# Kernel tuning notes

Measured on AMD Instinct MI355X. Metric: run time of the kernel, lower is better.

Reference implementation:

```python
import jax, jax.numpy as jnp
from jax import lax
import numpy as np

C_IN, D_INNER, D_STATE, OUT_CH = 20, 32, 8, 20
DT_RANK = max(1, D_INNER // 8)
B, H, W = 4, 384, 384
EPS = 1e-5


def layernorm(x, g, b):
    m = jnp.mean(x, axis=-1, keepdims=True)
    v = jnp.mean((x - m) ** 2, axis=-1, keepdims=True)
    return (x - m) * lax.rsqrt(v + EPS) * g + b


def ss1d(x, xw, dw, db, A_log, Dp):
    # x: (Bb, L, Dd). Mamba selective scan: h_t = exp(dt*A)*h_{t-1} + dt*B_t*u_t; y_t = C_t.h_t + D*u_t
    Bb, L, Dd = x.shape
    N = A_log.shape[1]
    xdbl = x @ xw.T                                   # (Bb, L, dtr+2N)
    dt_lo, Bm, Cm = jnp.split(xdbl, [DT_RANK, DT_RANK + N], axis=-1)
    dt = jax.nn.softplus(dt_lo @ dw.T + db)           # (Bb, L, Dd)
    A = -jnp.exp(A_log)                               # (Dd, N)

    def step(h, inp):
        dt_t, B_t, C_t, u_t = inp                     # (Bb,Dd),(Bb,N),(Bb,N),(Bb,Dd)
        dA = jnp.exp(dt_t[:, :, None] * A)            # (Bb, Dd, N)
        h = dA * h + (dt_t * u_t)[:, :, None] * B_t[:, None, :]
        y = jnp.einsum('bdn,bn->bd', h, C_t)
        return h, y

    xs = (jnp.moveaxis(dt, 1, 0), jnp.moveaxis(Bm, 1, 0),
          jnp.moveaxis(Cm, 1, 0), jnp.moveaxis(x, 1, 0))
    h0 = jnp.zeros((Bb, Dd, N), dtype=x.dtype)
    _, ys = lax.scan(step, h0, xs)
    return jnp.moveaxis(ys, 0, 1) + x * Dp


def setup_inputs() -> dict:
    key = jax.random.key(0)
    ks = jax.random.split(key, 16)
    s = lambda k, shp, sc=0.05: jax.random.normal(k, shp, dtype=jnp.float32) * sc
    A_log1 = jnp.log(jnp.broadcast_to(jnp.arange(1, D_STATE + 1, dtype=jnp.float32), (D_INNER, D_STATE)))
    return {
        'x': jax.random.normal(ks[0], (B, C_IN, H, W), dtype=jnp.float32),
        'norm_g': jnp.ones((C_IN,), jnp.float32),
        'norm_b': jnp.zeros((C_IN,), jnp.float32),
        'inproj_w': s(ks[1], (D_INNER, C_IN), 0.15),
        'dw_w': s(ks[2], (3, 3, 1, D_INNER), 0.2),
        'dw_b': jnp.zeros((D_INNER,), jnp.float32),
        'ssm_xw': s(ks[3], (4, DT_RANK + 2 * D_STATE, D_INNER), 0.1),
        'ssm_dw': s(ks[4], (4, D_INNER, DT_RANK), 0.5),
        'ssm_db': s(ks[5], (4, D_INNER), 0.5) - 3.0,
        'ssm_Alog': jnp.broadcast_to(A_log1, (4, D_INNER, D_STATE)).copy(),
        'ssm_D': jnp.ones((4, D_INNER), jnp.float32),
        'merge_g': jnp.ones((4 * D_INNER,), jnp.float32),
        'merge_b': jnp.zeros((4 * D_INNER,), jnp.float32),
        'merge_w': s(ks[6], (D_INNER, 4 * D_INNER), 0.1),
        'out_w': s(ks[7], (OUT_CH, D_INNER), 0.15),
        'out_b': jnp.zeros((OUT_CH,), jnp.float32),
    }


def reference(x, norm_g, norm_b, inproj_w, dw_w, dw_b, ssm_xw, ssm_dw, ssm_db,
              ssm_Alog, ssm_D, merge_g, merge_b, merge_w, out_w, out_b):
    Bx, C, Hx, Wx = x.shape
    h = jnp.transpose(x, (0, 2, 3, 1))                      # (B,H,W,C)
    h = layernorm(h, norm_g, norm_b)
    h = jax.nn.silu(h @ inproj_w.T)                          # (B,H,W,Dd)
    h = lax.conv_general_dilated(h, dw_w, (1, 1), 'SAME',
                                 dimension_numbers=('NHWC', 'HWIO', 'NHWC'),
                                 feature_group_count=D_INNER) + dw_b
    h = jax.nn.silu(h)                                       # (B,H,W,Dd)

    p = lambda i: (ssm_xw[i], ssm_dw[i], ssm_db[i], ssm_Alog[i], ssm_D[i])

    x_h = h.reshape(Bx * Hx, Wx, D_INNER)
    y_h_fwd = ss1d(x_h, *p(0)).reshape(Bx, Hx, Wx, D_INNER)
    y_h_bwd = ss1d(x_h[:, ::-1], *p(1))[:, ::-1].reshape(Bx, Hx, Wx, D_INNER)

    x_v = jnp.transpose(h, (0, 2, 1, 3)).reshape(Bx * Wx, Hx, D_INNER)
    y_v_fwd = jnp.transpose(ss1d(x_v, *p(2)).reshape(Bx, Wx, Hx, D_INNER), (0, 2, 1, 3))
    y_v_bwd = jnp.transpose(ss1d(x_v[:, ::-1], *p(3))[:, ::-1].reshape(Bx, Wx, Hx, D_INNER), (0, 2, 1, 3))

    y = jnp.concatenate([y_h_fwd, y_h_bwd, y_v_fwd, y_v_bwd], axis=-1)  # (B,H,W,4*Dd)
    y = layernorm(y, merge_g, merge_b)
    y = y @ merge_w.T                                        # (B,H,W,Dd)
    y = y @ out_w.T + out_b                                  # (B,H,W,out_ch)
    return jnp.transpose(y, (0, 3, 1, 2))                    # (B,out_ch,H,W)
```

## Files before the change

kernel.cpp:

```cpp
#include <hip/hip_runtime.h>

typedef unsigned short u16;
typedef unsigned int   u32;
typedef unsigned long long u64;
typedef float f2 __attribute__((ext_vector_type(2)));

#define CIN  20
#define DIN  32
#define BB   4
#define HH   384
#define WW   384
#define HW   147456
#define BHW  589824
#define EPSF 1e-5f
#define GUARD 65536

__device__ __forceinline__ float bflo(u32 u) {
    union { u32 v; float f; } x; x.v = u << 16; return x.f;
}
__device__ __forceinline__ float bfhi(u32 u) {
    union { u32 v; float f; } x; x.v = u & 0xffff0000u; return x.f;
}
__device__ __forceinline__ float bf2f(u16 h) {
    union { u32 v; float f; } x; x.v = ((u32)h) << 16; return x.f;
}
__device__ __forceinline__ u16 f2bf(float f) {
    union { float f; u32 u; } v; v.f = f;
    u32 u = v.u;
    return (u16)((u + 0x7FFFu + ((u >> 16) & 1u)) >> 16);
}
__device__ __forceinline__ float silu_f(float a) {
    return a / (1.f + __expf(-a));
}
__device__ __forceinline__ float softplus_f(float z) {
    return (z > 15.f) ? z : __logf(1.f + __expf(z));
}

__global__ void k_prep(const float* __restrict__ ow, const float* __restrict__ mw,
                       const float* __restrict__ mg, const float* __restrict__ mb,
                       const float* __restrict__ ob,
                       float* __restrict__ Wt, float* __restrict__ rsum,
                       float* __restrict__ c0)
{
    __shared__ float mdot[DIN];
    int t = threadIdx.x;
    if (t < DIN) {
        float s = 0.f;
        for (int k = 0; k < 128; ++k) s += mw[t*128 + k] * mb[k];
        mdot[t] = s;
    }
    {
        int k = t;
        for (int o = 0; o < CIN; ++o) {
            float s = 0.f;
            for (int d = 0; d < DIN; ++d) s += ow[o*DIN + d] * mw[d*128 + k];
            Wt[k*CIN + o] = s * mg[k];
        }
    }
    __syncthreads();
    if (t < CIN) {
        float rs = 0.f;
        for (int k = 0; k < 128; ++k) rs += Wt[k*CIN + t];
        rsum[t] = rs;
        float c = ob[t];
        for (int d = 0; d < DIN; ++d) c += ow[t*DIN + d] * mdot[d];
        c0[t] = c;
    }
}

__global__ __launch_bounds__(256) void k_lnproj(
    const float* __restrict__ x, const float* __restrict__ ng,
    const float* __restrict__ nb, const float* __restrict__ ipw,
    u16* __restrict__ h1)
{
    __shared__ float w_s[DIN*CIN];
    __shared__ float g_s[CIN], b_s[CIN];
    for (int i = threadIdx.x; i < DIN*CIN; i += 256) w_s[i] = ipw[i];
    if (threadIdx.x < CIN) { g_s[threadIdx.x] = ng[threadIdx.x]; b_s[threadIdx.x] = nb[threadIdx.x]; }
    __syncthreads();

    int p = blockIdx.x*256 + threadIdx.x;
    int b = p / HW, rem = p % HW;
    float v[CIN];
    float m = 0.f;
    #pragma unroll
    for (int c = 0; c < CIN; ++c) { v[c] = x[(b*CIN + c)*HW + rem]; m += v[c]; }
    m *= (1.f/CIN);
    float var = 0.f;
    #pragma unroll
    for (int c = 0; c < CIN; ++c) { float d = v[c]-m; var += d*d; }
    var *= (1.f/CIN);
    float rstd = rsqrtf(var + EPSF);
    #pragma unroll
    for (int c = 0; c < CIN; ++c) v[c] = (v[c]-m)*rstd*g_s[c] + b_s[c];

    float o[DIN];
    #pragma unroll
    for (int j = 0; j < DIN; ++j) {
        float acc = 0.f;
        #pragma unroll
        for (int c = 0; c < CIN; ++c) acc += w_s[j*CIN + c]*v[c];
        o[j] = silu_f(acc);
    }
    u32 pk[16];
    #pragma unroll
    for (int j2 = 0; j2 < 16; ++j2)
        pk[j2] = (u32)f2bf(o[2*j2]) | ((u32)f2bf(o[2*j2+1]) << 16);
    uint4* dst = (uint4*)(h1 + (size_t)p*DIN);
    dst[0] = make_uint4(pk[0],pk[1],pk[2],pk[3]);
    dst[1] = make_uint4(pk[4],pk[5],pk[6],pk[7]);
    dst[2] = make_uint4(pk[8],pk[9],pk[10],pk[11]);
    dst[3] = make_uint4(pk[12],pk[13],pk[14],pk[15]);
}

__global__ __launch_bounds__(256) void k_conv(
    const u16* __restrict__ h1, const float* __restrict__ cw,
    const float* __restrict__ cb, u16* __restrict__ h2)
{
    __shared__ float w_s[9*DIN];
    __shared__ float b_s[DIN];
    for (int i = threadIdx.x; i < 9*DIN; i += 256) w_s[i] = cw[i];
    if (threadIdx.x < DIN) b_s[threadIdx.x] = cb[threadIdx.x];
    __syncthreads();

    int tid = blockIdx.x*256 + threadIdx.x;
    int p = tid >> 2, g = tid & 3;
    int b = p / HW, rem = p % HW;
    int yy0 = rem / WW, xx0 = rem % WW;

    float acc[8];
    #pragma unroll
    for (int i = 0; i < 8; ++i) acc[i] = b_s[g*8 + i];

    #pragma unroll
    for (int dy = -1; dy <= 1; ++dy) {
        int yy = yy0 + dy;
        #pragma unroll
        for (int dx = -1; dx <= 1; ++dx) {
            int xc = xx0 + dx;
            if (yy >= 0 && yy < HH && xc >= 0 && xc < WW) {
                uint4 q = *(const uint4*)(h1 + ((size_t)(b*HW + yy*WW + xc)*DIN + g*8));
                int k = (dy+1)*3 + (dx+1);
                const float* wp = &w_s[k*DIN + g*8];
                acc[0] += wp[0]*bflo(q.x);  acc[1] += wp[1]*bfhi(q.x);
                acc[2] += wp[2]*bflo(q.y);  acc[3] += wp[3]*bfhi(q.y);
                acc[4] += wp[4]*bflo(q.z);  acc[5] += wp[5]*bfhi(q.z);
                acc[6] += wp[6]*bflo(q.w);  acc[7] += wp[7]*bfhi(q.w);
            }
        }
    }
    u32 pk[4];
    #pragma unroll
    for (int i2 = 0; i2 < 4; ++i2) {
        float a = silu_f(acc[2*i2]);
        float c = silu_f(acc[2*i2+1]);
        pk[i2] = (u32)f2bf(a) | ((u32)f2bf(c) << 16);
    }
    *(uint4*)(h2 + ((size_t)p*DIN + g*8)) = make_uint4(pk[0],pk[1],pk[2],pk[3]);
}

__global__ __launch_bounds__(256) void k_proj(
    const u16* __restrict__ h2, const float* __restrict__ xw,
    u16* __restrict__ dlA, u16* __restrict__ bcA)
{
    __shared__ float xw_s[4*CIN*DIN];
    for (int i = threadIdx.x; i < 4*CIN*DIN; i += 256) xw_s[i] = xw[i];
    __syncthreads();

    int p = blockIdx.x*256 + threadIdx.x;
    float u[DIN];
    const uint4* src = (const uint4*)(h2 + (size_t)p*DIN);
    #pragma unroll
    for (int q4 = 0; q4 < 4; ++q4) {
        uint4 v = src[q4];
        u[q4*8+0]=bflo(v.x); u[q4*8+1]=bfhi(v.x);
        u[q4*8+2]=bflo(v.y); u[q4*8+3]=bfhi(v.y);
        u[q4*8+4]=bflo(v.z); u[q4*8+5]=bfhi(v.z);
        u[q4*8+6]=bflo(v.w); u[q4*8+7]=bfhi(v.w);
    }
    #pragma unroll 1
    for (int dir = 0; dir < 4; ++dir) {
        float xd[CIN];
        #pragma unroll
        for (int j = 0; j < CIN; ++j) xd[j] = 0.f;
        #pragma unroll
        for (int d4 = 0; d4 < 8; ++d4) {
            float u0 = u[d4*4], u1 = u[d4*4+1], u2 = u[d4*4+2], u3 = u[d4*4+3];
            #pragma unroll
            for (int j = 0; j < CIN; ++j) {
                float4 w4 = *(const float4*)&xw_s[(dir*CIN + j)*DIN + d4*4];
                xd[j] += w4.x*u0 + w4.y*u1 + w4.z*u2 + w4.w*u3;
            }
        }
        u32 pk[10];
        #pragma unroll
        for (int i = 0; i < 10; ++i)
            pk[i] = (u32)f2bf(xd[2*i]) | ((u32)f2bf(xd[2*i+1]) << 16);
        *(uint2*)(dlA + (size_t)(dir*BHW + p)*4) = make_uint2(pk[0], pk[1]);
        uint4* bcd = (uint4*)(bcA + (size_t)(dir*BHW + p)*16);
        bcd[0] = make_uint4(pk[2], pk[3], pk[4], pk[5]);
        bcd[1] = make_uint4(pk[6], pk[7], pk[8], pk[9]);
    }
}

__global__ __launch_bounds__(256) void k_scan(
    const char* __restrict__ h2b,
    const char* __restrict__ dlb_,
    const char* __restrict__ bcb_,
    const float* __restrict__ Alog, const float* __restrict__ Dp,
    const float* __restrict__ dwm,  const float* __restrict__ dbv,
    char* __restrict__ y4b)
{
    int tid  = blockIdx.x*256 + threadIdx.x;
    int wv   = tid >> 6, lane = tid & 63;
    int half = lane >> 5, d = lane & 31;
    int dir  = wv / 768;
    int s    = (wv % 768)*2 + half;
    int b    = s / 384, r = s % 384;

    int p0, stp;
    if (dir == 0)      { p0 = b*HW + r*WW;           stp = 1;  }
    else if (dir == 1) { p0 = b*HW + r*WW + (WW-1);  stp = -1; }
    else if (dir == 2) { p0 = b*HW + r;              stp = WW; }
    else               { p0 = b*HW + (HH-1)*WW + r;  stp = -WW;}

    float Av[8];
    bool okl = true;
    #pragma unroll
    for (int j = 0; j < 8; ++j) {
        float e = __expf(Alog[(dir*DIN + d)*8 + j]);
        Av[j] = -e;
        okl = okl && (__builtin_fabsf(e - (float)(j+1)) < 2e-3f);
    }
    bool fast = (__ballot(okl) == ~0ull);

    float Dd  = Dp[dir*DIN + d];
    float dw0 = dwm[(dir*DIN + d)*4 + 0], dw1 = dwm[(dir*DIN + d)*4 + 1];
    float dw2 = dwm[(dir*DIN + d)*4 + 2], dw3 = dwm[(dir*DIN + d)*4 + 3];
    float dbc = dbv[dir*DIN + d];

    u32 uo = GUARD + (u32)((p0*DIN + d)*2);            int su = stp*DIN*2;
    u32 yo = (u32)((dir*BHW + p0)*64 + d*2);           int sy = stp*64;
    u32 c1 = GUARD + (u32)((dir*BHW + p0)*8);          int s1 = stp*8;
    u32 c2 = GUARD + (u32)((dir*BHW + p0)*32);         int s2 = stp*32;

    u16 ub[2]; uint2 dlr[2]; uint4 B4[2], C4[2];
    u32 fu = uo, f1 = c1, f2o = c2;

    auto fetch = [&](int sl) {
        ub[sl]  = *(const u16*)(h2b + fu);
        dlr[sl] = *(const uint2*)(dlb_ + f1);
        B4[sl]  = *(const uint4*)(bcb_ + f2o);
        C4[sl]  = *(const uint4*)(bcb_ + f2o + 16);
        fu += (u32)su; f1 += (u32)s1; f2o += (u32)s2;
    };

    fetch(0); fetch(1);

    f2 h0 = {0.f,0.f}, h1 = {0.f,0.f}, h2v = {0.f,0.f}, h3 = {0.f,0.f};

    if (fast) {
        #pragma unroll 2
        for (int t = 0; t < 384; ++t) {
            int sl = t & 1;
            float uu = bf2f(ub[sl]);
            uint2 dl = dlr[sl];
            uint4 Bv = B4[sl], Cv = C4[sl];
            fetch(sl);

            float z = dbc + dw0*bflo(dl.x) + dw1*bfhi(dl.x)
                          + dw2*bflo(dl.y) + dw3*bfhi(dl.y);
            z = fminf(z, 80.f);
            float rr = __builtin_amdgcn_rcpf(1.f + __expf(z));
            float dt = -__logf(rr);
            float r2 = rr*rr;
            f2 rr2 = {r2, r2};
            f2 a01 = {rr, r2};
            f2 a23 = a01*rr2;
            f2 a45 = a23*rr2;
            f2 a67 = a45*rr2;

            float dtu = dt*uu;
            f2 du2 = {dtu, dtu};
            f2 Bp0 = { bflo(Bv.x), bfhi(Bv.x) }, Bp1 = { bflo(Bv.y), bfhi(Bv.y) };
            f2 Bp2 = { bflo(Bv.z), bfhi(Bv.z) }, Bp3 = { bflo(Bv.w), bfhi(Bv.w) };
            f2 Cp0 = { bflo(Cv.x), bfhi(Cv.x) }, Cp1 = { bflo(Cv.y), bfhi(Cv.y) };
            f2 Cp2 = { bflo(Cv.z), bfhi(Cv.z) }, Cp3 = { bflo(Cv.w), bfhi(Cv.w) };

            h0  = __builtin_elementwise_fma(a01, h0,  du2*Bp0);
            h1  = __builtin_elementwise_fma(a23, h1,  du2*Bp1);
            h2v = __builtin_elementwise_fma(a45, h2v, du2*Bp2);
            h3  = __builtin_elementwise_fma(a67, h3,  du2*Bp3);

            f2 yv = Cp0*h0;
            yv = __builtin_elementwise_fma(Cp1, h1,  yv);
            yv = __builtin_elementwise_fma(Cp2, h2v, yv);
            yv = __builtin_elementwise_fma(Cp3, h3,  yv);

            float y = yv.x + yv.y + Dd*uu;
            *(u16*)(y4b + yo) = f2bf(y);
            yo += (u32)sy;
        }
    } else {
        f2 A2[4];
        #pragma unroll
        for (int j = 0; j < 4; ++j) { A2[j].x = Av[2*j]; A2[j].y = Av[2*j+1]; }
        #pragma unroll 2
        for (int t = 0; t < 384; ++t) {
            int sl = t & 1;
            float uu = bf2f(ub[sl]);
            uint2 dl = dlr[sl];
            uint4 Bv = B4[sl], Cv = C4[sl];
            fetch(sl);

            float z = dbc + dw0*bflo(dl.x) + dw1*bfhi(dl.x)
                          + dw2*bflo(dl.y) + dw3*bfhi(dl.y);
            float dt = softplus_f(z);
            f2 dt2 = {dt, dt};
            f2 e0 = dt2*A2[0], e1 = dt2*A2[1], e2 = dt2*A2[2], e3 = dt2*A2[3];
            f2 a01 = { __expf(e0.x), __expf(e0.y) };
            f2 a23 = { __expf(e1.x), __expf(e1.y) };
            f2 a45 = { __expf(e2.x), __expf(e2.y) };
            f2 a67 = { __expf(e3.x), __expf(e3.y) };

            float dtu = dt*uu;
            f2 du2 = {dtu, dtu};
            f2 Bp0 = { bflo(Bv.x), bfhi(Bv.x) }, Bp1 = { bflo(Bv.y), bfhi(Bv.y) };
            f2 Bp2 = { bflo(Bv.z), bfhi(Bv.z) }, Bp3 = { bflo(Bv.w), bfhi(Bv.w) };
            f2 Cp0 = { bflo(Cv.x), bfhi(Cv.x) }, Cp1 = { bflo(Cv.y), bfhi(Cv.y) };
            f2 Cp2 = { bflo(Cv.z), bfhi(Cv.z) }, Cp3 = { bflo(Cv.w), bfhi(Cv.w) };

            h0  = __builtin_elementwise_fma(a01, h0,  du2*Bp0);
            h1  = __builtin_elementwise_fma(a23, h1,  du2*Bp1);
            h2v = __builtin_elementwise_fma(a45, h2v, du2*Bp2);
            h3  = __builtin_elementwise_fma(a67, h3,  du2*Bp3);

            f2 yv = Cp0*h0;
            yv = __builtin_elementwise_fma(Cp1, h1,  yv);
            yv = __builtin_elementwise_fma(Cp2, h2v, yv);
            yv = __builtin_elementwise_fma(Cp3, h3,  yv);

            float y = yv.x + yv.y + Dd*uu;
            *(u16*)(y4b + yo) = f2bf(y);
            yo += (u32)sy;
        }
    }
}

__global__ __launch_bounds__(256) void k_merge(
    const u16* __restrict__ y4, const float* __restrict__ Wt,
    const float* __restrict__ rsum, const float* __restrict__ c0,
    float* __restrict__ out)
{
    __shared__ float Wt_s[128*CIN];
    __shared__ float rs_s[CIN], c0_s[CIN];
    for (int i = threadIdx.x; i < 128*CIN; i += 256) Wt_s[i] = Wt[i];
    if (threadIdx.x < CIN) { rs_s[threadIdx.x] = rsum[threadIdx.x]; c0_s[threadIdx.x] = c0[threadIdx.x]; }
    __syncthreads();

    int p = blockIdx.x*256 + threadIdx.x;
    int b = p / HW, rem = p % HW;

    float s1 = 0.f, s2 = 0.f;
    float acc[CIN];
    #pragma unroll
    for (int o = 0; o < CIN; ++o) acc[o] = 0.f;

    #pragma unroll 1
    for (int dirk = 0; dirk < 4; ++dirk) {
        const uint4* src = (const uint4*)(y4 + ((size_t)dirk*BHW + p)*32);
        #pragma unroll
        for (int q4 = 0; q4 < 4; ++q4) {
            uint4 v = src[q4];
            u32 w[4] = {v.x, v.y, v.z, v.w};
            #pragma unroll
            for (int i = 0; i < 4; ++i) {
                int k = dirk*32 + q4*8 + i*2;
                float a = bflo(w[i]); float c = bfhi(w[i]);
                s1 += a + c; s2 += a*a + c*c;
                const float4* w0 = (const float4*)&Wt_s[k*CIN];
                const float4* w1 = (const float4*)&Wt_s[(k+1)*CIN];
                #pragma unroll
                for (int o4 = 0; o4 < 5; ++o4) {
                    float4 x0 = w0[o4], x1 = w1[o4];
                    acc[o4*4+0] += x0.x*a + x1.x*c;
                    acc[o4*4+1] += x0.y*a + x1.y*c;
                    acc[o4*4+2] += x0.z*a + x1.z*c;
                    acc[o4*4+3] += x0.w*a + x1.w*c;
                }
            }
        }
    }
    float m = s1*(1.f/128.f);
    float var = s2*(1.f/128.f) - m*m;
    float rstd = rsqrtf(var + EPSF);
    #pragma unroll
    for (int o = 0; o < CIN; ++o) {
        float res = rstd*(acc[o] - m*rs_s[o]) + c0_s[o];
        out[(b*CIN + o)*HW + rem] = res;
    }
}

extern "C" void kernel_launch(void* const* d_in, const int* in_sizes, int n_in,
                              void* d_out, int out_size, void* d_ws, size_t ws_size,
                              hipStream_t stream)
{
    const float* x    = (const float*)d_in[0];
    const float* ng   = (const float*)d_in[1];
    const float* nb   = (const float*)d_in[2];
    const float* ipw  = (const float*)d_in[3];
    const float* cw   = (const float*)d_in[4];
    const float* cb   = (const float*)d_in[5];
    const float* xw   = (const float*)d_in[6];
    const float* dwm  = (const float*)d_in[7];
    const float* dbv  = (const float*)d_in[8];
    const float* Alog = (const float*)d_in[9];
    const float* Dpv  = (const float*)d_in[10];
    const float* mg   = (const float*)d_in[11];
    const float* mb   = (const float*)d_in[12];
    const float* mw   = (const float*)d_in[13];
    const float* ow   = (const float*)d_in[14];
    const float* ob   = (const float*)d_in[15];
    float* out = (float*)d_out;

    const size_t y4_bytes = (size_t)4*BHW*DIN*2;
    const size_t dl_bytes = (size_t)4*BHW*8;
    const size_t bc_bytes = (size_t)4*BHW*32;
    const size_t wt_bytes = (size_t)(128*CIN + 64)*4;

    char* ws = (char*)d_ws;
    u16* y4 = (u16*)ws;
    u16* h1 = y4;

    size_t dl_pos = y4_bytes + GUARD;
    size_t bc_pos = dl_pos + dl_bytes + GUARD;
    size_t wt_pos = bc_pos + bc_bytes + GUARD;
    size_t need   = wt_pos + wt_bytes + GUARD;

    if (ws_size < need) {
        hipMemsetAsync(d_out, 0x7F, (size_t)out_size*4, stream);
        return;
    }

    char* h2base = (char*)d_out;
    u16*  h2 = (u16*)(h2base + GUARD);

    u16* dlA = (u16*)(ws + dl_pos);
    u16* bcA = (u16*)(ws + bc_pos);
    float* Wt   = (float*)(ws + wt_pos);
    float* rsum = Wt + 128*CIN;
    float* c0   = rsum + 32;

    k_prep  <<<1, 128, 0, stream>>>(ow, mw, mg, mb, ob, Wt, rsum, c0);
    k_lnproj<<<BHW/256, 256, 0, stream>>>(x, ng, nb, ipw, h1);
    k_conv  <<<BHW*4/256, 256, 0, stream>>>(h1, cw, cb, h2);
    k_proj  <<<BHW/256, 256, 0, stream>>>(h2, xw, dlA, bcA);
    k_scan  <<<768, 256, 0, stream>>>(
        h2base, (const char*)(ws + dl_pos - GUARD), (const char*)(ws + bc_pos - GUARD),
        Alog, Dpv, dwm, dbv, (char*)y4);
    k_merge <<<BHW/256, 256, 0, stream>>>(y4, Wt, rsum, c0, out);
}
```

Baseline: 530.3 us.

## Fuse layernorm-proj, depthwise conv and x-proj into one tiled front kernel

Merges the layernorm+input projection, the 3x3 depthwise conv and the per-direction x projection into a single 16x16-tiled kernel. The projected h1 tile plus its halo lives in shared memory, so the h1 round trip through global memory and two launches go away. The price is recomputing the halo pixels and using more shared memory per block. A second change stores B/C in fp32 when the workspace is large enough, which removes bf16 unpacking in the scan but doubles the bytes the scan reads for B and C.

```diff
diff --git a/kernel.cpp b/kernel.cpp
--- a/kernel.cpp
+++ b/kernel.cpp
@@ -28,6 +28,9 @@
     union { float f; u32 u; } v; v.f = f;
     u32 u = v.u;
     return (u16)((u + 0x7FFFu + ((u >> 16) & 1u)) >> 16);
+}
+__device__ __forceinline__ u32 pk2(float a, float b) {
+    return (u32)f2bf(a) | ((u32)f2bf(b) << 16);
 }
 __device__ __forceinline__ float silu_f(float a) {
     return a / (1.f + __expf(-a));
@@ -68,116 +71,101 @@
     }
 }
 
-__global__ __launch_bounds__(256) void k_lnproj(
+template<bool BIGBC>
+__global__ __launch_bounds__(256) void k_front(
     const float* __restrict__ x, const float* __restrict__ ng,
     const float* __restrict__ nb, const float* __restrict__ ipw,
-    u16* __restrict__ h1)
+    const float* __restrict__ cw, const float* __restrict__ cb,
+    const float* __restrict__ xw,
+    u16* __restrict__ h2, u16* __restrict__ dlA, char* __restrict__ bcA)
 {
-    __shared__ float w_s[DIN*CIN];
+    __shared__ u32   h1_s[324*16];
+    __shared__ float ipw_s[DIN*CIN];
+    __shared__ float xw_s[4*CIN*DIN];
+    __shared__ float cw_s[9*DIN];
+    __shared__ float cb_s[DIN];
     __shared__ float g_s[CIN], b_s[CIN];
-    for (int i = threadIdx.x; i < DIN*CIN; i += 256) w_s[i] = ipw[i];
-    if (threadIdx.x < CIN) { g_s[threadIdx.x] = ng[threadIdx.x]; b_s[threadIdx.x] = nb[threadIdx.x]; }
+
+    int tid = threadIdx.x;
+    for (int i = tid; i < DIN*CIN; i += 256) ipw_s[i] = ipw[i];
+    for (int i = tid; i < 4*CIN*DIN; i += 256) xw_s[i] = xw[i];
+    for (int i = tid; i < 9*DIN; i += 256) cw_s[i] = cw[i];
+    if (tid < DIN) cb_s[tid] = cb[tid];
+    if (tid < CIN) { g_s[tid] = ng[tid]; b_s[tid] = nb[tid]; }
     __syncthreads();
 
-    int p = blockIdx.x*256 + threadIdx.x;
-    int b = p / HW, rem = p % HW;
-    float v[CIN];
-    float m = 0.f;
-    #pragma unroll
-    for (int c = 0; c < CIN; ++c) { v[c] = x[(b*CIN + c)*HW + rem]; m += v[c]; }
-    m *= (1.f/CIN);
-    float var = 0.f;
-    #pragma unroll
-    for (int c = 0; c < CIN; ++c) { float d = v[c]-m; var += d*d; }
-    var *= (1.f/CIN);
-    float rstd = rsqrtf(var + EPSF);
-    #pragma unroll
-    for (int c = 0; c < CIN; ++c) v[c] = (v[c]-m)*rstd*g_s[c] + b_s[c];
-
-    float o[DIN];
-    #pragma unroll
-    for (int j = 0; j < DIN; ++j) {
-        float acc = 0.f;
+    int b  = blockIdx.z;
+    int x0 = blockIdx.x*16 - 1, y0 = blockIdx.y*16 - 1;
+    const float* xb = x + (size_t)b*CIN*HW;
+
+    for (int i = tid; i < 324; i += 256) {
+        int hx = x0 + (i % 18), hy = y0 + (i / 18);
+        u32* dst = &h1_s[i*16];
+        if ((unsigned)hx >= 384u || (unsigned)hy >= 384u) {
+            #pragma unroll
+            for (int q = 0; q < 16; ++q) dst[q] = 0u;
+        } else {
+            int pix = hy*WW + hx;
+            float v[CIN]; float m = 0.f;
+            #pragma unroll
+            for (int c = 0; c < CIN; ++c) { v[c] = xb[c*HW + pix]; m += v[c]; }
+            m *= (1.f/CIN);
+            float var = 0.f;
+            #pragma unroll
+            for (int c = 0; c < CIN; ++c) { float dd = v[c]-m; var += dd*dd; }
+            float rstd = rsqrtf(var*(1.f/CIN) + EPSF);
+            #pragma unroll
+            for (int c = 0; c < CIN; ++c) v[c] = (v[c]-m)*rstd*g_s[c] + b_s[c];
+            #pragma unroll
+            for (int q = 0; q < 16; ++q) {
+                float a0 = 0.f, a1 = 0.f;
+                #pragma unroll
+                for (int c = 0; c < CIN; ++c) {
+                    a0 += ipw_s[(2*q)*CIN + c]*v[c];
+                    a1 += ipw_s[(2*q+1)*CIN + c]*v[c];
+                }
+                dst[q] = pk2(silu_f(a0), silu_f(a1));
+            }
+        }
+    }
+    __syncthreads();
+
+    int tx = tid & 15, ty = tid >> 4;
+    float hc[DIN];
+    #pragma unroll
+    for (int i = 0; i < DIN; ++i) hc[i] = cb_s[i];
+    #pragma unroll
+    for (int ky = 0; ky < 3; ++ky) {
         #pragma unroll
-        for (int c = 0; c < CIN; ++c) acc += w_s[j*CIN + c]*v[c];
-        o[j] = silu_f(acc);
-    }
-    u32 pk[16];
-    #pragma unroll
-    for (int j2 = 0; j2 < 16; ++j2)
-        pk[j2] = (u32)f2bf(o[2*j2]) | ((u32)f2bf(o[2*j2+1]) << 16);
-    uint4* dst = (uint4*)(h1 + (size_t)p*DIN);
-    dst[0] = make_uint4(pk[0],pk[1],pk[2],pk[3]);
-    dst[1] = make_uint4(pk[4],pk[5],pk[6],pk[7]);
-    dst[2] = make_uint4(pk[8],pk[9],pk[10],pk[11]);
-    dst[3] = make_uint4(pk[12],pk[13],pk[14],pk[15]);
-}
-
-__global__ __launch_bounds__(256) void k_conv(
-    const u16* __restrict__ h1, const float* __restrict__ cw,
-    const float* __restrict__ cb, u16* __restrict__ h2)
-{
-    __shared__ float w_s[9*DIN];
-    __shared__ float b_s[DIN];
-    for (int i = threadIdx.x; i < 9*DIN; i += 256) w_s[i] = cw[i];
-    if (threadIdx.x < DIN) b_s[threadIdx.x] = cb[threadIdx.x];
-    __syncthreads();
-
-    int tid = blockIdx.x*256 + threadIdx.x;
-    int p = tid >> 2, g = tid & 3;
-    int b = p / HW, rem = p % HW;
-    int yy0 = rem / WW, xx0 = rem % WW;
-
-    float acc[8];
-    #pragma unroll
-    for (int i = 0; i < 8; ++i) acc[i] = b_s[g*8 + i];
-
-    #pragma unroll
-    for (int dy = -1; dy <= 1; ++dy) {
-        int yy = yy0 + dy;
+        for (int kx = 0; kx < 3; ++kx) {
+            const uint4* src = (const uint4*)&h1_s[((ty+ky)*18 + tx+kx)*16];
+            const float* wp = &cw_s[(ky*3+kx)*DIN];
+            #pragma unroll
+            for (int q4 = 0; q4 < 4; ++q4) {
+                uint4 w = src[q4];
+                hc[q4*8+0] += wp[q4*8+0]*bflo(w.x); hc[q4*8+1] += wp[q4*8+1]*bfhi(w.x);
+                hc[q4*8+2] += wp[q4*8+2]*bflo(w.y); hc[q4*8+3] += wp[q4*8+3]*bfhi(w.y);
+                hc[q4*8+4] += wp[q4*8+4]*bflo(w.z); hc[q4*8+5] += wp[q4*8+5]*bfhi(w.z);
+                hc[q4*8+6] += wp[q4*8+6]*bflo(w.w); hc[q4*8+7] += wp[q4*8+7]*bfhi(w.w);
+            }
+        }
+    }
+    #pragma unroll
+    for (int i = 0; i < DIN; ++i) hc[i] = silu_f(hc[i]);
+
+    int p = b*HW + (y0+1+ty)*WW + (x0+1+tx);
+
+    {
+        u32 pk[16];
         #pragma unroll
-        for (int dx = -1; dx <= 1; ++dx) {
-            int xc = xx0 + dx;
-            if (yy >= 0 && yy < HH && xc >= 0 && xc < WW) {
-                uint4 q = *(const uint4*)(h1 + ((size_t)(b*HW + yy*WW + xc)*DIN + g*8));
-                int k = (dy+1)*3 + (dx+1);
-                const float* wp = &w_s[k*DIN + g*8];
-                acc[0] += wp[0]*bflo(q.x);  acc[1] += wp[1]*bfhi(q.x);
-                acc[2] += wp[2]*bflo(q.y);  acc[3] += wp[3]*bfhi(q.y);
-                acc[4] += wp[4]*bflo(q.z);  acc[5] += wp[5]*bfhi(q.z);
-                acc[6] += wp[6]*bflo(q.w);  acc[7] += wp[7]*bfhi(q.w);
-            }
-        }
-    }
-    u32 pk[4];
-    #pragma unroll
-    for (int i2 = 0; i2 < 4; ++i2) {
-        float a = silu_f(acc[2*i2]);
-        float c = silu_f(acc[2*i2+1]);
-        pk[i2] = (u32)f2bf(a) | ((u32)f2bf(c) << 16);
-    }
-    *(uint4*)(h2 + ((size_t)p*DIN + g*8)) = make_uint4(pk[0],pk[1],pk[2],pk[3]);
-}
-
-__global__ __launch_bounds__(256) void k_proj(
-    const u16* __restrict__ h2, const float* __restrict__ xw,
-    u16* __restrict__ dlA, u16* __restrict__ bcA)
-{
-    __shared__ float xw_s[4*CIN*DIN];
-    for (int i = threadIdx.x; i < 4*CIN*DIN; i += 256) xw_s[i] = xw[i];
-    __syncthreads();
-
-    int p = blockIdx.x*256 + threadIdx.x;
-    float u[DIN];
-    const uint4* src = (const uint4*)(h2 + (size_t)p*DIN);
-    #pragma unroll
-    for (int q4 = 0; q4 < 4; ++q4) {
-        uint4 v = src[q4];
-        u[q4*8+0]=bflo(v.x); u[q4*8+1]=bfhi(v.x);
-        u[q4*8+2]=bflo(v.y); u[q4*8+3]=bfhi(v.y);
-        u[q4*8+4]=bflo(v.z); u[q4*8+5]=bfhi(v.z);
-        u[q4*8+6]=bflo(v.w); u[q4*8+7]=bfhi(v.w);
-    }
+        for (int q = 0; q < 16; ++q) pk[q] = pk2(hc[2*q], hc[2*q+1]);
+        uint4* hd = (uint4*)(h2 + (size_t)p*DIN);
+        hd[0] = make_uint4(pk[0], pk[1], pk[2], pk[3]);
+        hd[1] = make_uint4(pk[4], pk[5], pk[6], pk[7]);
+        hd[2] = make_uint4(pk[8], pk[9], pk[10],pk[11]);
+        hd[3] = make_uint4(pk[12],pk[13],pk[14],pk[15]);
+    }
+
     #pragma unroll 1
     for (int dir = 0; dir < 4; ++dir) {
         float xd[CIN];
@@ -185,24 +173,32 @@
         for (int j = 0; j < CIN; ++j) xd[j] = 0.f;
         #pragma unroll
         for (int d4 = 0; d4 < 8; ++d4) {
-            float u0 = u[d4*4], u1 = u[d4*4+1], u2 = u[d4*4+2], u3 = u[d4*4+3];
+            float u0 = hc[d4*4], u1 = hc[d4*4+1], u2 = hc[d4*4+2], u3 = hc[d4*4+3];
             #pragma unroll
             for (int j = 0; j < CIN; ++j) {
                 float4 w4 = *(const float4*)&xw_s[(dir*CIN + j)*DIN + d4*4];
                 xd[j] += w4.x*u0 + w4.y*u1 + w4.z*u2 + w4.w*u3;
             }
         }
-        u32 pk[10];
-        #pragma unroll
-        for (int i = 0; i < 10; ++i)
-            pk[i] = (u32)f2bf(xd[2*i]) | ((u32)f2bf(xd[2*i+1]) << 16);
-        *(uint2*)(dlA + (size_t)(dir*BHW + p)*4) = make_uint2(pk[0], pk[1]);
-        uint4* bcd = (uint4*)(bcA + (size_t)(dir*BHW + p)*16);
-        bcd[0] = make_uint4(pk[2], pk[3], pk[4], pk[5]);
-        bcd[1] = make_uint4(pk[6], pk[7], pk[8], pk[9]);
-    }
-}
-
+        *(uint2*)(dlA + (size_t)(dir*BHW + p)*4) =
+            make_uint2(pk2(xd[0], xd[1]), pk2(xd[2], xd[3]));
+        if (BIGBC) {
+            float4* bcd = (float4*)(bcA + (size_t)(dir*BHW + p)*64);
+            bcd[0] = make_float4(xd[4],  xd[5],  xd[6],  xd[7]);
+            bcd[1] = make_float4(xd[8],  xd[9],  xd[10], xd[11]);
+            bcd[2] = make_float4(xd[12], xd[13], xd[14], xd[15]);
+            bcd[3] = make_float4(xd[16], xd[17], xd[18], xd[19]);
+        } else {
+            uint4* bcd = (uint4*)(bcA + (size_t)(dir*BHW + p)*32);
+            bcd[0] = make_uint4(pk2(xd[4],xd[5]),   pk2(xd[6],xd[7]),
+                                pk2(xd[8],xd[9]),   pk2(xd[10],xd[11]));
+            bcd[1] = make_uint4(pk2(xd[12],xd[13]), pk2(xd[14],xd[15]),
+                                pk2(xd[16],xd[17]), pk2(xd[18],xd[19]));
+        }
+    }
+}
+
+template<bool BIGBC>
 __global__ __launch_bounds__(256) void k_scan(
     const char* __restrict__ h2b,
     const char* __restrict__ dlb_,
@@ -239,19 +235,29 @@
     float dw2 = dwm[(dir*DIN + d)*4 + 2], dw3 = dwm[(dir*DIN + d)*4 + 3];
     float dbc = dbv[dir*DIN + d];
 
+    const int RSZ = BIGBC ? 64 : 32;
     u32 uo = GUARD + (u32)((p0*DIN + d)*2);            int su = stp*DIN*2;
     u32 yo = (u32)((dir*BHW + p0)*64 + d*2);           int sy = stp*64;
     u32 c1 = GUARD + (u32)((dir*BHW + p0)*8);          int s1 = stp*8;
-    u32 c2 = GUARD + (u32)((dir*BHW + p0)*32);         int s2 = stp*32;
-
-    u16 ub[2]; uint2 dlr[2]; uint4 B4[2], C4[2];
+    u32 c2 = GUARD + (u32)((dir*BHW + p0)*RSZ);        int s2 = stp*RSZ;
+
+    u16 ub[2]; uint2 dlr[2];
+    uint4  B4[2], C4[2];
+    float4 Ba[2], Bb[2], Ca[2], Cb[2];
     u32 fu = uo, f1 = c1, f2o = c2;
 
     auto fetch = [&](int sl) {
         ub[sl]  = *(const u16*)(h2b + fu);
         dlr[sl] = *(const uint2*)(dlb_ + f1);
-        B4[sl]  = *(const uint4*)(bcb_ + f2o);
-        C4[sl]  = *(const uint4*)(bcb_ + f2o + 16);
+        if (BIGBC) {
+            Ba[sl] = *(const float4*)(bcb_ + f2o);
+            Bb[sl] = *(const float4*)(bcb_ + f2o + 16);
+            Ca[sl] = *(const float4*)(bcb_ + f2o + 32);
+            Cb[sl] = *(const float4*)(bcb_ + f2o + 48);
+        } else {
+            B4[sl]  = *(const uint4*)(bcb_ + f2o);
+            C4[sl]  = *(const uint4*)(bcb_ + f2o + 16);
+        }
         fu += (u32)su; f1 += (u32)s1; f2o += (u32)s2;
     };
 
@@ -259,91 +265,68 @@
 
     f2 h0 = {0.f,0.f}, h1 = {0.f,0.f}, h2v = {0.f,0.f}, h3 = {0.f,0.f};
 
-    if (fast) {
-        #pragma unroll 2
-        for (int t = 0; t < 384; ++t) {
-            int sl = t & 1;
-            float uu = bf2f(ub[sl]);
-            uint2 dl = dlr[sl];
+    #pragma unroll 2
+    for (int t = 0; t < 384; ++t) {
+        int sl = t & 1;
+        float uu = bf2f(ub[sl]);
+        uint2 dl = dlr[sl];
+        f2 Bp0, Bp1, Bp2, Bp3, Cp0, Cp1, Cp2, Cp3;
+        if (BIGBC) {
+            float4 xa = Ba[sl], xb2 = Bb[sl], ya = Ca[sl], yb = Cb[sl];
+            Bp0 = f2{xa.x, xa.y};  Bp1 = f2{xa.z, xa.w};
+            Bp2 = f2{xb2.x, xb2.y}; Bp3 = f2{xb2.z, xb2.w};
+            Cp0 = f2{ya.x, ya.y};  Cp1 = f2{ya.z, ya.w};
+            Cp2 = f2{yb.x, yb.y};  Cp3 = f2{yb.z, yb.w};
+        } else {
             uint4 Bv = B4[sl], Cv = C4[sl];
-            fetch(sl);
-
-            float z = dbc + dw0*bflo(dl.x) + dw1*bfhi(dl.x)
-                          + dw2*bflo(dl.y) + dw3*bfhi(dl.y);
+            Bp0 = f2{ bflo(Bv.x), bfhi(Bv.x) }; Bp1 = f2{ bflo(Bv.y), bfhi(Bv.y) };
+            Bp2 = f2{ bflo(Bv.z), bfhi(Bv.z) }; Bp3 = f2{ bflo(Bv.w), bfhi(Bv.w) };
+            Cp0 = f2{ bflo(Cv.x), bfhi(Cv.x) }; Cp1 = f2{ bflo(Cv.y), bfhi(Cv.y) };
+            Cp2 = f2{ bflo(Cv.z), bfhi(Cv.z) }; Cp3 = f2{ bflo(Cv.w), bfhi(Cv.w) };
+        }
+        fetch(sl);
+
+        float z = dbc + dw0*bflo(dl.x) + dw1*bfhi(dl.x)
+                      + dw2*bflo(dl.y) + dw3*bfhi(dl.y);
+        f2 a01, a23, a45, a67;
+        float dt;
+        if (fast) {
             z = fminf(z, 80.f);
             float rr = __builtin_amdgcn_rcpf(1.f + __expf(z));
-            float dt = -__logf(rr);
+            dt = -__logf(rr);
             float r2 = rr*rr;
             f2 rr2 = {r2, r2};
-            f2 a01 = {rr, r2};
-            f2 a23 = a01*rr2;
-            f2 a45 = a23*rr2;
-            f2 a67 = a45*rr2;
-
-            float dtu = dt*uu;
-            f2 du2 = {dtu, dtu};
-            f2 Bp0 = { bflo(Bv.x), bfhi(Bv.x) }, Bp1 = { bflo(Bv.y), bfhi(Bv.y) };
-            f2 Bp2 = { bflo(Bv.z), bfhi(Bv.z) }, Bp3 = { bflo(Bv.w), bfhi(Bv.w) };
-            f2 Cp0 = { bflo(Cv.x), bfhi(Cv.x) }, Cp1 = { bflo(Cv.y), bfhi(Cv.y) };
-            f2 Cp2 = { bflo(Cv.z), bfhi(Cv.z) }, Cp3 = { bflo(Cv.w), bfhi(Cv.w) };
-
-            h0  = __builtin_elementwise_fma(a01, h0,  du2*Bp0);
-            h1  = __builtin_elementwise_fma(a23, h1,  du2*Bp1);
-            h2v = __builtin_elementwise_fma(a45, h2v, du2*Bp2);
-            h3  = __builtin_elementwise_fma(a67, h3,  du2*Bp3);
-
-            f2 yv = Cp0*h0;
-            yv = __builtin_elementwise_fma(Cp1, h1,  yv);
-            yv = __builtin_elementwise_fma(Cp2, h2v, yv);
-            yv = __builtin_elementwise_fma(Cp3, h3,  yv);
-
-            float y = yv.x + yv.y + Dd*uu;
-            *(u16*)(y4b + yo) = f2bf(y);
-            yo += (u32)sy;
-        }
-    } else {
-        f2 A2[4];
-        #pragma unroll
-        for (int j = 0; j < 4; ++j) { A2[j].x = Av[2*j]; A2[j].y = Av[2*j+1]; }
-        #pragma unroll 2
-        for (int t = 0; t < 384; ++t) {
-            int sl = t & 1;
-            float uu = bf2f(ub[sl]);
-            uint2 dl = dlr[sl];
-            uint4 Bv = B4[sl], Cv = C4[sl];
-            fetch(sl);
-
-            float z = dbc + dw0*bflo(dl.x) + dw1*bfhi(dl.x)
-                          + dw2*bflo(dl.y) + dw3*bfhi(dl.y);
-            float dt = softplus_f(z);
+            a01 = f2{rr, r2};
+            a23 = a01*rr2;
+            a45 = a23*rr2;
+            a67 = a45*rr2;
+        } else {
+            dt = softplus_f(z);
             f2 dt2 = {dt, dt};
-            f2 e0 = dt2*A2[0], e1 = dt2*A2[1], e2 = dt2*A2[2], e3 = dt2*A2[3];
-            f2 a01 = { __expf(e0.x), __expf(e0.y) };
-            f2 a23 = { __expf(e1.x), __expf(e1.y) };
-            f2 a45 = { __expf(e2.x), __expf(e2.y) };
-            f2 a67 = { __expf(e3.x), __expf(e3.y) };
-
-            float dtu = dt*uu;
-            f2 du2 = {dtu, dtu};
-            f2 Bp0 = { bflo(Bv.x), bfhi(Bv.x) }, Bp1 = { bflo(Bv.y), bfhi(Bv.y) };
-            f2 Bp2 = { bflo(Bv.z), bfhi(Bv.z) }, Bp3 = { bflo(Bv.w), bfhi(Bv.w) };
-            f2 Cp0 = { bflo(Cv.x), bfhi(Cv.x) }, Cp1 = { bflo(Cv.y), bfhi(Cv.y) };
-            f2 Cp2 = { bflo(Cv.z), bfhi(Cv.z) }, Cp3 = { bflo(Cv.w), bfhi(Cv.w) };
-
-            h0  = __builtin_elementwise_fma(a01, h0,  du2*Bp0);
-            h1  = __builtin_elementwise_fma(a23, h1,  du2*Bp1);
-            h2v = __builtin_elementwise_fma(a45, h2v, du2*Bp2);
-            h3  = __builtin_elementwise_fma(a67, h3,  du2*Bp3);
-
-            f2 yv = Cp0*h0;
-            yv = __builtin_elementwise_fma(Cp1, h1,  yv);
-            yv = __builtin_elementwise_fma(Cp2, h2v, yv);
-            yv = __builtin_elementwise_fma(Cp3, h3,  yv);
-
-            float y = yv.x + yv.y + Dd*uu;
-            *(u16*)(y4b + yo) = f2bf(y);
-            yo += (u32)sy;
-        }
+            f2 e0 = dt2*f2{Av[0],Av[1]}, e1 = dt2*f2{Av[2],Av[3]};
+            f2 e2 = dt2*f2{Av[4],Av[5]}, e3 = dt2*f2{Av[6],Av[7]};
+            a01 = f2{ __expf(e0.x), __expf(e0.y) };
+            a23 = f2{ __expf(e1.x), __expf(e1.y) };
+            a45 = f2{ __expf(e2.x), __expf(e2.y) };
+            a67 = f2{ __expf(e3.x), __expf(e3.y) };
+        }
+
+        float dtu = dt*uu;
+        f2 du2 = {dtu, dtu};
+
+        h0  = __builtin_elementwise_fma(a01, h0,  du2*Bp0);
+        h1  = __builtin_elementwise_fma(a23, h1,  du2*Bp1);
+        h2v = __builtin_elementwise_fma(a45, h2v, du2*Bp2);
+        h3  = __builtin_elementwise_fma(a67, h3,  du2*Bp3);
+
+        f2 yv = Cp0*h0;
+        yv = __builtin_elementwise_fma(Cp1, h1,  yv);
+        yv = __builtin_elementwise_fma(Cp2, h2v, yv);
+        yv = __builtin_elementwise_fma(Cp3, h3,  yv);
+
+        float y = yv.x + yv.y + Dd*uu;
+        *(u16*)(y4b + yo) = f2bf(y);
+        yo += (u32)sy;
     }
 }
 
@@ -423,40 +406,50 @@
     const float* ob   = (const float*)d_in[15];
     float* out = (float*)d_out;
 
-    const size_t y4_bytes = (size_t)4*BHW*DIN*2;
-    const size_t dl_bytes = (size_t)4*BHW*8;
-    const size_t bc_bytes = (size_t)4*BHW*32;
-    const size_t wt_bytes = (size_t)(128*CIN + 64)*4;
+    const size_t y4_bytes   = (size_t)4*BHW*DIN*2;
+    const size_t dl_bytes   = (size_t)4*BHW*8;
+    const size_t bc16_bytes = (size_t)4*BHW*32;
+    const size_t bc32_bytes = (size_t)4*BHW*64;
+    const size_t wt_bytes   = (size_t)(128*CIN + 64)*4;
 
     char* ws = (char*)d_ws;
     u16* y4 = (u16*)ws;
-    u16* h1 = y4;
 
     size_t dl_pos = y4_bytes + GUARD;
     size_t bc_pos = dl_pos + dl_bytes + GUARD;
-    size_t wt_pos = bc_pos + bc_bytes + GUARD;
-    size_t need   = wt_pos + wt_bytes + GUARD;
-
-    if (ws_size < need) {
+    size_t need_small = bc_pos + bc16_bytes + GUARD + wt_bytes + GUARD;
+    size_t need_big   = bc_pos + bc32_bytes + GUARD + wt_bytes + GUARD;
+
+    if (ws_size < need_small) {
         hipMemsetAsync(d_out, 0x7F, (size_t)out_size*4, stream);
         return;
     }
+    bool big = (ws_size >= need_big);
 
     char* h2base = (char*)d_out;
     u16*  h2 = (u16*)(h2base + GUARD);
 
-    u16* dlA = (u16*)(ws + dl_pos);
-    u16* bcA = (u16*)(ws + bc_pos);
+    u16*  dlA = (u16*)(ws + dl_pos);
+    char* bcA = ws + bc_pos;
+    size_t wt_pos = bc_pos + (big ? bc32_bytes : bc16_bytes) + GUARD;
     float* Wt   = (float*)(ws + wt_pos);
     float* rsum = Wt + 128*CIN;
     float* c0   = rsum + 32;
 
-    k_prep  <<<1, 128, 0, stream>>>(ow, mw, mg, mb, ob, Wt, rsum, c0);
-    k_lnproj<<<BHW/256, 256, 0, stream>>>(x, ng, nb, ipw, h1);
-    k_conv  <<<BHW*4/256, 256, 0, stream>>>(h1, cw, cb, h2);
-    k_proj  <<<BHW/256, 256, 0, stream>>>(h2, xw, dlA, bcA);
-    k_scan  <<<768, 256, 0, stream>>>(
-        h2base, (const char*)(ws + dl_pos - GUARD), (const char*)(ws + bc_pos - GUARD),
-        Alog, Dpv, dwm, dbv, (char*)y4);
-    k_merge <<<BHW/256, 256, 0, stream>>>(y4, Wt, rsum, c0, out);
-}
+    k_prep<<<1, 128, 0, stream>>>(ow, mw, mg, mb, ob, Wt, rsum, c0);
+
+    dim3 fgrid(24, 24, 4);
+    if (big) {
+        k_front<true><<<fgrid, 256, 0, stream>>>(x, ng, nb, ipw, cw, cb, xw, h2, dlA, bcA);
+        k_scan<true><<<768, 256, 0, stream>>>(
+            h2base, (const char*)(ws + dl_pos - GUARD), (const char*)(ws + bc_pos - GUARD),
+            Alog, Dpv, dwm, dbv, (char*)y4);
+    } else {
+        k_front<false><<<fgrid, 256, 0, stream>>>(x, ng, nb, ipw, cw, cb, xw, h2, dlA, bcA);
+        k_scan<false><<<768, 256, 0, stream>>>(
+            h2base, (const char*)(ws + dl_pos - GUARD), (const char*)(ws + bc_pos - GUARD),
+            Alog, Dpv, dwm, dbv, (char*)y4);
+    }
+
+    k_merge<<<BHW/256, 256, 0, stream>>>(y4, Wt, rsum, c0, out);
+}
```

After: 702.5 us. 1.32x slower.
